# Kernel tuning notes

Measured on AMD Instinct MI355X. Metric: run time of the kernel, lower is better.

Reference implementation:

```python
import jax, jax.numpy as jnp
import numpy as np

N_NODES = 50000
N_EDGES = 800000
N_GRAPHS = 512
VOCAB = 128
HID = 64
NCLS = 5


def _seg_mean(vals, ids, num_segments):
    s = jax.ops.segment_sum(vals, ids, num_segments=num_segments)
    cnt = jax.ops.segment_sum(jnp.ones((vals.shape[0],), vals.dtype), ids, num_segments=num_segments)
    return s / jnp.maximum(cnt, 1.0)[:, None]


def sage_conv(x, src, dst, W_l, b_l, W_r):
    # PyG SAGEConv (mean aggr): out = lin_l(mean_{j in N(i)} x_j) + lin_r(x_i)
    agg = _seg_mean(x[src], dst, x.shape[0])          # [N, H] gather + scatter-mean
    return agg @ W_l.T + b_l + x @ W_r.T


def setup_inputs() -> dict:
    key = jax.random.key(0)
    ks = jax.random.split(key, 10)
    scale = 1.0 / np.sqrt(HID)
    x_tokens = jax.random.randint(ks[0], (N_NODES,), 0, VOCAB)
    edge_index = jax.random.randint(ks[1], (2, N_EDGES), 0, N_NODES)
    batch = jnp.sort(jax.random.randint(ks[2], (N_NODES,), 0, N_GRAPHS))
    return {
        "x_tokens": x_tokens,
        "edge_index": edge_index,
        "batch": batch,
        "embed": jax.random.normal(ks[3], (VOCAB, HID), jnp.float32),
        "W1l": jax.random.normal(ks[4], (HID, HID), jnp.float32) * scale,
        "b1l": jnp.zeros((HID,), jnp.float32),
        "W1r": jax.random.normal(ks[5], (HID, HID), jnp.float32) * scale,
        "W2l": jax.random.normal(ks[6], (HID, HID), jnp.float32) * scale,
        "b2l": jnp.zeros((HID,), jnp.float32),
        "W2r": jax.random.normal(ks[7], (HID, HID), jnp.float32) * scale,
        "Wlin": jax.random.normal(ks[8], (NCLS, HID), jnp.float32) * scale,
        "blin": jnp.zeros((NCLS,), jnp.float32),
    }


def reference(x_tokens, edge_index, batch, embed, W1l, b1l, W1r, W2l, b2l, W2r, Wlin, blin):
    src, dst = edge_index[0], edge_index[1]
    x = embed[x_tokens]                                  # [N, H] embedding lookup
    x = jax.nn.relu(sage_conv(x, src, dst, W1l, b1l, W1r))
    x = jax.nn.relu(sage_conv(x, src, dst, W2l, b2l, W2r))
    g = _seg_mean(x, batch, N_GRAPHS)                    # global_mean_pool -> [G, H]
    return g @ Wlin.T + blin                             # [G, num_classes]
```

## Files before the change

kernel.cpp:

```cpp
#include <hip/hip_runtime.h>

#define N_NODES  50000
#define N_EDGES  800000
#define N_GRAPHS 512
#define HID      64
#define NCLS     5
#define NB       64
#define EST      36
#define AST      68

typedef __attribute__((ext_vector_type(8))) short bf16x8;
typedef __attribute__((ext_vector_type(4))) float f32x4;

__device__ inline unsigned short f2bf(float f) {
    unsigned int u = __builtin_bit_cast(unsigned int, f);
    unsigned int r = (u + 0x7FFFu + ((u >> 16) & 1u)) >> 16;
    return (unsigned short)r;
}
__device__ inline unsigned int packbf(float a, float b) {
    return (unsigned int)f2bf(a) | ((unsigned int)f2bf(b) << 16);
}
__device__ inline float bf2f(unsigned int u16) {
    unsigned int t = u16 << 16;
    return __builtin_bit_cast(float, t);
}

#define EBUF_T (128 * 32)
#define PW_T   (64 * 64)
#define PREP_T (N_EDGES + EBUF_T + N_NODES + 2 * PW_T)
__global__ void k_prep_fill(
    const int* __restrict__ src, const int* __restrict__ dst,
    const int* __restrict__ tok,
    int* __restrict__ cnt, unsigned int* __restrict__ bucket,
    const float* __restrict__ embed, unsigned int* __restrict__ ebufg,
    const int* __restrict__ batch,
    int* __restrict__ pos_start, int* __restrict__ pos_end,
    const float* __restrict__ W1l, const float* __restrict__ W1r,
    unsigned int* __restrict__ wb1,
    const float* __restrict__ W2l, const float* __restrict__ W2r,
    unsigned int* __restrict__ wb2) {
    int gid = blockIdx.x * blockDim.x + threadIdx.x;
    if (gid < N_EDGES) {
        int s = src[gid], d = dst[gid];
        unsigned int t = (unsigned int)tok[s];
        int pos = atomicAdd(&cnt[d], 1);
        if (pos < NB) {
            __builtin_nontemporal_store((unsigned int)s | (t << 16),
                                        &bucket[(long)d * NB + pos]);
        }
        return;
    }
    gid -= N_EDGES;
    if (gid < EBUF_T) {
        int t = gid >> 5, c = gid & 31;
        float2 v = ((const float2*)(embed + (long)t * HID))[c];
        ebufg[gid] = packbf(v.x, v.y);
        return;
    }
    gid -= EBUF_T;
    if (gid < N_NODES) {
        int n = gid;
        int b = batch[n];
        if (n == 0 || batch[n - 1] != b) pos_start[b] = n;
        if (n == N_NODES - 1 || batch[n + 1] != b) pos_end[b] = n + 1;
        return;
    }
    gid -= N_NODES;
    if (gid < 2 * PW_T) {
        const float* Wl = (gid < PW_T) ? W1l : W2l;
        const float* Wr = (gid < PW_T) ? W1r : W2r;
        unsigned int* wb = (gid < PW_T) ? wb1 : wb2;
        int i = (gid < PW_T) ? gid : gid - PW_T;
        int h = i >> 6, c = i & 63;
        float2 v = (c < 32) ? ((const float2*)(Wl + (long)h * HID))[c]
                            : ((const float2*)(Wr + (long)h * HID))[c - 32];
        wb[i] = packbf(v.x, v.y);
    }
}

template <bool L1>
__global__ __launch_bounds__(1024) void k_layer(
    const int* __restrict__ cnt, const unsigned int* __restrict__ bucket,
    const int* __restrict__ tok, const unsigned int* __restrict__ ebufg,
    const unsigned int* __restrict__ xb,
    const unsigned int* __restrict__ wb, const float* __restrict__ bl,
    unsigned short* __restrict__ xoutb)
{
    __shared__ unsigned int As[64 * AST];
    __shared__ unsigned int elds[L1 ? 128 * EST : 1];
    const int tid  = threadIdx.x;
    const int wv   = tid >> 6;
    const int lane = tid & 63;
    const int n0   = blockIdx.x * 64;

    if (L1) {
        for (int i = tid; i < EBUF_T; i += 1024) {
            int t = i >> 5, c = i & 31;
            elds[t * EST + c] = ebufg[i];
        }
        __syncthreads();
    }

    const int q  = lane & 7;
    const int e8 = lane >> 3;

#pragma unroll
    for (int i = 0; i < 4; ++i) {
        int rl = wv * 4 + i;
        int nn = n0 + rl;
        int nc = min(nn, N_NODES - 1);
        int deg = cnt[nc];
        int m   = (nn < N_NODES) ? min(deg, NB) : 0;
        unsigned int v = (lane < m) ? bucket[(long)nc * NB + lane] : 0u;
        float f0 = 0, f1 = 0, f2 = 0, f3 = 0, f4 = 0, f5 = 0, f6 = 0, f7 = 0;
#pragma unroll
        for (int g = 0; g < 8; ++g) {
            int j = g * 8 + e8;
            unsigned int vv = __shfl(v, j, 64);
            if (j < m) {
                uint4 w4;
                if (L1) w4 = *(const uint4*)(elds + (vv >> 16) * EST + q * 4);
                else    w4 = *((const uint4*)(xb + (long)(vv & 0xffffu) * 32) + q);
                f0 += bf2f(w4.x & 0xffff); f1 += bf2f(w4.x >> 16);
                f2 += bf2f(w4.y & 0xffff); f3 += bf2f(w4.y >> 16);
                f4 += bf2f(w4.z & 0xffff); f5 += bf2f(w4.z >> 16);
                f6 += bf2f(w4.w & 0xffff); f7 += bf2f(w4.w >> 16);
            }
        }
#pragma unroll
        for (int o = 8; o < 64; o <<= 1) {
            f0 += __shfl_xor(f0, o, 64); f1 += __shfl_xor(f1, o, 64);
            f2 += __shfl_xor(f2, o, 64); f3 += __shfl_xor(f3, o, 64);
            f4 += __shfl_xor(f4, o, 64); f5 += __shfl_xor(f5, o, 64);
            f6 += __shfl_xor(f6, o, 64); f7 += __shfl_xor(f7, o, 64);
        }
        if (e8 == 0) {
            float inv = 1.0f / (float)max(deg, 1);
            uint4 o;
            o.x = packbf(f0 * inv, f1 * inv);
            o.y = packbf(f2 * inv, f3 * inv);
            o.z = packbf(f4 * inv, f5 * inv);
            o.w = packbf(f6 * inv, f7 * inv);
            *(uint4*)(As + rl * AST + q * 4) = o;
        } else if (e8 == 1) {
            uint4 sv;
            if (L1) { int tk = tok[nc]; sv = *(const uint4*)(elds + tk * EST + q * 4); }
            else    { sv = *((const uint4*)(xb + (long)nc * 32) + q); }
            *(uint4*)(As + rl * AST + 32 + q * 4) = sv;
        }
    }
    __syncthreads();

    const int s    = wv & 3;
    const int t    = wv >> 2;
    const int mm   = lane & 15;
    const int quad = lane >> 4;

    bf16x8 afr[4];
#pragma unroll
    for (int kst = 0; kst < 4; ++kst)
        afr[kst] = *(const bf16x8*)(As + (s * 16 + mm) * AST + kst * 16 + quad * 4);

    f32x4 acc = (f32x4){0.f, 0.f, 0.f, 0.f};
#pragma unroll
    for (int kst = 0; kst < 4; ++kst) {
        bf16x8 bfr = *(const bf16x8*)(wb + (t * 16 + mm) * 64 + kst * 16 + quad * 4);
        acc = __builtin_amdgcn_mfma_f32_16x16x32_bf16(bfr, afr[kst], acc, 0, 0, 0);
    }

    int node = n0 + s * 16 + mm;
    if (node < N_NODES) {
        int hb = t * 16 + quad * 4;
        float4 bb = *(const float4*)(bl + hb);
        ushort4 o;
        o.x = f2bf(fmaxf(acc[0] + bb.x, 0.f));
        o.y = f2bf(fmaxf(acc[1] + bb.y, 0.f));
        o.z = f2bf(fmaxf(acc[2] + bb.z, 0.f));
        o.w = f2bf(fmaxf(acc[3] + bb.w, 0.f));
        *(ushort4*)(xoutb + (long)node * HID + hb) = o;
    }
}

__global__ __launch_bounds__(64) void k_pool(
    const unsigned int* __restrict__ x2b,
    const int* __restrict__ pos_start, const int* __restrict__ pos_end,
    const float* __restrict__ Wlin, const float* __restrict__ blin,
    float* __restrict__ out)
{
    int g    = blockIdx.x;
    int lane = threadIdx.x;
    int q    = lane & 7;
    int slot = lane >> 3;
    int s = pos_start[g], e = pos_end[g];
    float f0 = 0, f1 = 0, f2 = 0, f3 = 0, f4 = 0, f5 = 0, f6 = 0, f7 = 0;
    for (int n = s + slot; n < e; n += 8) {
        uint4 v = *((const uint4*)(x2b + (long)n * 32) + q);
        f0 += bf2f(v.x & 0xffff); f1 += bf2f(v.x >> 16);
        f2 += bf2f(v.y & 0xffff); f3 += bf2f(v.y >> 16);
        f4 += bf2f(v.z & 0xffff); f5 += bf2f(v.z >> 16);
        f6 += bf2f(v.w & 0xffff); f7 += bf2f(v.w >> 16);
    }
#pragma unroll
    for (int o = 8; o < 64; o <<= 1) {
        f0 += __shfl_xor(f0, o, 64); f1 += __shfl_xor(f1, o, 64);
        f2 += __shfl_xor(f2, o, 64); f3 += __shfl_xor(f3, o, 64);
        f4 += __shfl_xor(f4, o, 64); f5 += __shfl_xor(f5, o, 64);
        f6 += __shfl_xor(f6, o, 64); f7 += __shfl_xor(f7, o, 64);
    }
    float inv = 1.0f / (float)max(e - s, 1);
    f0 *= inv; f1 *= inv; f2 *= inv; f3 *= inv;
    f4 *= inv; f5 *= inv; f6 *= inv; f7 *= inv;
#pragma unroll
    for (int c = 0; c < NCLS; ++c) {
        const float* wr = Wlin + c * HID + q * 8;
        float p = f0 * wr[0] + f1 * wr[1] + f2 * wr[2] + f3 * wr[3] +
                  f4 * wr[4] + f5 * wr[5] + f6 * wr[6] + f7 * wr[7];
        p += __shfl_xor(p, 1, 64);
        p += __shfl_xor(p, 2, 64);
        p += __shfl_xor(p, 4, 64);
        if (lane == 0) out[g * NCLS + c] = p + blin[c];
    }
}

extern "C" void kernel_launch(void* const* d_in, const int* in_sizes, int n_in,
                              void* d_out, int out_size, void* d_ws, size_t ws_size,
                              hipStream_t stream) {
    const int*   tok   = (const int*)d_in[0];
    const int*   eidx  = (const int*)d_in[1];
    const int*   batch = (const int*)d_in[2];
    const float* embed = (const float*)d_in[3];
    const float* W1l   = (const float*)d_in[4];
    const float* b1l   = (const float*)d_in[5];
    const float* W1r   = (const float*)d_in[6];
    const float* W2l   = (const float*)d_in[7];
    const float* b2l   = (const float*)d_in[8];
    const float* W2r   = (const float*)d_in[9];
    const float* Wlin  = (const float*)d_in[10];
    const float* blin  = (const float*)d_in[11];
    float* out = (float*)d_out;

    const int* src = eidx;
    const int* dst = eidx + N_EDGES;

    char* wsp = (char*)d_ws;
    size_t off = 0;
    auto alloc = [&](size_t bytes) -> void* {
        void* p = wsp + off;
        off = (off + bytes + 255) & ~(size_t)255;
        return p;
    };
    int*   cnt     = (int*)  alloc((size_t)N_NODES * 4);
    int*   pstart  = (int*)  alloc((size_t)N_GRAPHS * 4);
    int*   pend    = (int*)  alloc((size_t)N_GRAPHS * 4);
    unsigned int* bucket = (unsigned int*)alloc((size_t)N_NODES * NB * 4);
    unsigned int* x1b    = (unsigned int*)alloc((size_t)N_NODES * 32 * 4);
    unsigned int* x2b    = (unsigned int*)alloc((size_t)N_NODES * 32 * 4);
    unsigned int* ebufg  = (unsigned int*)alloc((size_t)128 * 32 * 4);
    unsigned int* wb1    = (unsigned int*)alloc((size_t)64 * 64 * 4);
    unsigned int* wb2    = (unsigned int*)alloc((size_t)64 * 64 * 4);

    hipMemsetAsync(cnt, 0, (char*)pend - (char*)cnt + (size_t)N_GRAPHS * 4, stream);

    k_prep_fill<<<(PREP_T + 255) / 256, 256, 0, stream>>>(
        src, dst, tok, cnt, bucket,
        embed, ebufg, batch, pstart, pend, W1l, W1r, wb1, W2l, W2r, wb2);

    const int LBLK = (N_NODES + 63) / 64;
    k_layer<true><<<LBLK, 1024, 0, stream>>>(cnt, bucket, tok, ebufg, nullptr,
                                             wb1, b1l, (unsigned short*)x1b);
    k_layer<false><<<LBLK, 1024, 0, stream>>>(cnt, bucket, nullptr, nullptr, x1b,
                                              wb2, b2l, (unsigned short*)x2b);

    k_pool<<<N_GRAPHS, 64, 0, stream>>>(x2b, pstart, pend, Wlin, blin, out);
}
```

Baseline: 214.0 us.

## Replace per-node global atomic bucketing with two-pass binned counting sort

Instead of each edge doing a global atomicAdd on its destination node's counter and writing into a padded 50000x64 bucket array, edges are histogrammed per 64-node bin in shared memory, scanned, and scattered into a compact per-bin edge list. Each layer block then rebuilds its 64 node buckets in LDS from that bin's edges. This is meant to remove heavy global atomic contention and the large sparse bucket footprint. The cost is two extra kernel launches, including a single-block scan, and rebuilding the LDS buckets in both layers.

After: 226.9 us. 1.06x slower.

```diff
diff --git a/kernel.cpp b/kernel.cpp
--- a/kernel.cpp
+++ b/kernel.cpp
@@ -5,7 +5,9 @@
 #define N_GRAPHS 512
 #define HID      64
 #define NCLS     5
-#define NB       64
+#define NBIN     782
+#define BB       64
+#define EPB      (N_EDGES / BB)
 #define EST      36
 #define AST      68
 
@@ -27,11 +29,10 @@
 
 #define EBUF_T (128 * 32)
 #define PW_T   (64 * 64)
-#define PREP_T (N_EDGES + EBUF_T + N_NODES + 2 * PW_T)
-__global__ void k_prep_fill(
-    const int* __restrict__ src, const int* __restrict__ dst,
-    const int* __restrict__ tok,
-    int* __restrict__ cnt, unsigned int* __restrict__ bucket,
+#define PREP_T (EBUF_T + N_NODES + 2 * PW_T)
+#define PREP_B ((PREP_T + 255) / 256)
+__global__ __launch_bounds__(256) void k_prep_bin1(
+    const int* __restrict__ dst, int* __restrict__ hist,
     const float* __restrict__ embed, unsigned int* __restrict__ ebufg,
     const int* __restrict__ batch,
     int* __restrict__ pos_start, int* __restrict__ pos_end,
@@ -39,18 +40,19 @@
     unsigned int* __restrict__ wb1,
     const float* __restrict__ W2l, const float* __restrict__ W2r,
     unsigned int* __restrict__ wb2) {
-    int gid = blockIdx.x * blockDim.x + threadIdx.x;
-    if (gid < N_EDGES) {
-        int s = src[gid], d = dst[gid];
-        unsigned int t = (unsigned int)tok[s];
-        int pos = atomicAdd(&cnt[d], 1);
-        if (pos < NB) {
-            __builtin_nontemporal_store((unsigned int)s | (t << 16),
-                                        &bucket[(long)d * NB + pos]);
-        }
+    __shared__ int h[NBIN];
+    if (blockIdx.x < BB) {
+        for (int i = threadIdx.x; i < NBIN; i += 256) h[i] = 0;
+        __syncthreads();
+        int base = blockIdx.x * EPB;
+        for (int i = threadIdx.x; i < EPB; i += 256)
+            atomicAdd(&h[dst[base + i] >> 6], 1);
+        __syncthreads();
+        for (int i = threadIdx.x; i < NBIN; i += 256)
+            hist[blockIdx.x * NBIN + i] = h[i];
         return;
     }
-    gid -= N_EDGES;
+    int gid = (blockIdx.x - BB) * 256 + threadIdx.x;
     if (gid < EBUF_T) {
         int t = gid >> 5, c = gid & 31;
         float2 v = ((const float2*)(embed + (long)t * HID))[c];
@@ -71,35 +73,103 @@
         const float* Wr = (gid < PW_T) ? W1r : W2r;
         unsigned int* wb = (gid < PW_T) ? wb1 : wb2;
         int i = (gid < PW_T) ? gid : gid - PW_T;
-        int h = i >> 6, c = i & 63;
-        float2 v = (c < 32) ? ((const float2*)(Wl + (long)h * HID))[c]
-                            : ((const float2*)(Wr + (long)h * HID))[c - 32];
+        int h2 = i >> 6, c = i & 63;
+        float2 v = (c < 32) ? ((const float2*)(Wl + (long)h2 * HID))[c]
+                            : ((const float2*)(Wr + (long)h2 * HID))[c - 32];
         wb[i] = packbf(v.x, v.y);
+    }
+}
+
+__global__ __launch_bounds__(1024) void k_scan(
+    const int* __restrict__ hist, int* __restrict__ bbase,
+    int* __restrict__ bin_off, int* __restrict__ bin_cnt) {
+    __shared__ int sh[1024];
+    int j = threadIdx.x;
+    int run = 0;
+    if (j < NBIN) {
+#pragma unroll 8
+        for (int b = 0; b < BB; ++b) {
+            bbase[b * NBIN + j] = run;
+            run += hist[b * NBIN + j];
+        }
+    }
+    sh[j] = (j < NBIN) ? run : 0;
+    __syncthreads();
+    for (int o = 1; o < 1024; o <<= 1) {
+        int t = (j >= o) ? sh[j - o] : 0;
+        __syncthreads();
+        sh[j] += t;
+        __syncthreads();
+    }
+    if (j < NBIN) {
+        int off = sh[j] - run;
+        bin_off[j] = off;
+        bin_cnt[j] = run;
+#pragma unroll 8
+        for (int b = 0; b < BB; ++b) bbase[b * NBIN + j] += off;
+    }
+}
+
+__global__ __launch_bounds__(256) void k_bin2(
+    const int* __restrict__ src, const int* __restrict__ dst,
+    const int* __restrict__ tok, const int* __restrict__ bbase,
+    unsigned int* __restrict__ ebin) {
+    __shared__ int base[NBIN];
+    __shared__ int cur[NBIN];
+    for (int i = threadIdx.x; i < NBIN; i += 256) {
+        base[i] = bbase[blockIdx.x * NBIN + i];
+        cur[i] = 0;
+    }
+    __syncthreads();
+    int eb = blockIdx.x * EPB;
+    for (int i = threadIdx.x; i < EPB; i += 256) {
+        int s = src[eb + i], d = dst[eb + i];
+        unsigned int t = (unsigned int)tok[s];
+        int bin = d >> 6;
+        int pos = atomicAdd(&cur[bin], 1);
+        ebin[base[bin] + pos] =
+            (unsigned int)s | ((unsigned int)(d & 63) << 16) | (t << 22);
     }
 }
 
 template <bool L1>
 __global__ __launch_bounds__(1024) void k_layer(
-    const int* __restrict__ cnt, const unsigned int* __restrict__ bucket,
+    const int* __restrict__ bin_off, const int* __restrict__ bin_cnt,
+    const unsigned int* __restrict__ ebin,
     const int* __restrict__ tok, const unsigned int* __restrict__ ebufg,
     const unsigned int* __restrict__ xb,
     const unsigned int* __restrict__ wb, const float* __restrict__ bl,
     unsigned short* __restrict__ xoutb)
 {
     __shared__ unsigned int As[64 * AST];
+    __shared__ unsigned int lbucket[64 * 64];
+    __shared__ int lcnt[64];
     __shared__ unsigned int elds[L1 ? 128 * EST : 1];
     const int tid  = threadIdx.x;
     const int wv   = tid >> 6;
     const int lane = tid & 63;
     const int n0   = blockIdx.x * 64;
 
+    if (tid < 64) lcnt[tid] = 0;
     if (L1) {
         for (int i = tid; i < EBUF_T; i += 1024) {
             int t = i >> 5, c = i & 31;
             elds[t * EST + c] = ebufg[i];
         }
-        __syncthreads();
-    }
+    }
+    __syncthreads();
+
+    {
+        int boffv = bin_off[blockIdx.x];
+        int bcnt  = bin_cnt[blockIdx.x];
+        for (int i = tid; i < bcnt; i += 1024) {
+            unsigned int v = ebin[boffv + i];
+            int dl = (v >> 16) & 63;
+            int pos = atomicAdd(&lcnt[dl], 1);
+            if (pos < 64) lbucket[dl * 64 + pos] = v;
+        }
+    }
+    __syncthreads();
 
     const int q  = lane & 7;
     const int e8 = lane >> 3;
@@ -109,9 +179,9 @@
         int rl = wv * 4 + i;
         int nn = n0 + rl;
         int nc = min(nn, N_NODES - 1);
-        int deg = cnt[nc];
-        int m   = (nn < N_NODES) ? min(deg, NB) : 0;
-        unsigned int v = (lane < m) ? bucket[(long)nc * NB + lane] : 0u;
+        int deg = lcnt[rl];
+        int m   = min(deg, 64);
+        unsigned int v = (lane < m) ? lbucket[rl * 64 + lane] : 0u;
         float f0 = 0, f1 = 0, f2 = 0, f3 = 0, f4 = 0, f5 = 0, f6 = 0, f7 = 0;
 #pragma unroll
         for (int g = 0; g < 8; ++g) {
@@ -119,7 +189,7 @@
             unsigned int vv = __shfl(v, j, 64);
             if (j < m) {
                 uint4 w4;
-                if (L1) w4 = *(const uint4*)(elds + (vv >> 16) * EST + q * 4);
+                if (L1) w4 = *(const uint4*)(elds + (vv >> 22) * EST + q * 4);
                 else    w4 = *((const uint4*)(xb + (long)(vv & 0xffffu) * 32) + q);
                 f0 += bf2f(w4.x & 0xffff); f1 += bf2f(w4.x >> 16);
                 f2 += bf2f(w4.y & 0xffff); f3 += bf2f(w4.y >> 16);
@@ -249,27 +319,33 @@
         off = (off + bytes + 255) & ~(size_t)255;
         return p;
     };
-    int*   cnt     = (int*)  alloc((size_t)N_NODES * 4);
     int*   pstart  = (int*)  alloc((size_t)N_GRAPHS * 4);
     int*   pend    = (int*)  alloc((size_t)N_GRAPHS * 4);
-    unsigned int* bucket = (unsigned int*)alloc((size_t)N_NODES * NB * 4);
-    unsigned int* x1b    = (unsigned int*)alloc((size_t)N_NODES * 32 * 4);
-    unsigned int* x2b    = (unsigned int*)alloc((size_t)N_NODES * 32 * 4);
-    unsigned int* ebufg  = (unsigned int*)alloc((size_t)128 * 32 * 4);
-    unsigned int* wb1    = (unsigned int*)alloc((size_t)64 * 64 * 4);
-    unsigned int* wb2    = (unsigned int*)alloc((size_t)64 * 64 * 4);
-
-    hipMemsetAsync(cnt, 0, (char*)pend - (char*)cnt + (size_t)N_GRAPHS * 4, stream);
-
-    k_prep_fill<<<(PREP_T + 255) / 256, 256, 0, stream>>>(
-        src, dst, tok, cnt, bucket,
-        embed, ebufg, batch, pstart, pend, W1l, W1r, wb1, W2l, W2r, wb2);
-
-    const int LBLK = (N_NODES + 63) / 64;
-    k_layer<true><<<LBLK, 1024, 0, stream>>>(cnt, bucket, tok, ebufg, nullptr,
-                                             wb1, b1l, (unsigned short*)x1b);
-    k_layer<false><<<LBLK, 1024, 0, stream>>>(cnt, bucket, nullptr, nullptr, x1b,
-                                              wb2, b2l, (unsigned short*)x2b);
+    int*   hist    = (int*)  alloc((size_t)BB * NBIN * 4);
+    int*   bbase   = (int*)  alloc((size_t)BB * NBIN * 4);
+    int*   bin_off = (int*)  alloc((size_t)NBIN * 4);
+    int*   bin_cnt = (int*)  alloc((size_t)NBIN * 4);
+    unsigned int* ebin  = (unsigned int*)alloc((size_t)N_EDGES * 4);
+    unsigned int* x1b   = (unsigned int*)alloc((size_t)N_NODES * 32 * 4);
+    unsigned int* x2b   = (unsigned int*)alloc((size_t)N_NODES * 32 * 4);
+    unsigned int* ebufg = (unsigned int*)alloc((size_t)128 * 32 * 4);
+    unsigned int* wb1   = (unsigned int*)alloc((size_t)64 * 64 * 4);
+    unsigned int* wb2   = (unsigned int*)alloc((size_t)64 * 64 * 4);
+
+    hipMemsetAsync(pstart, 0, (char*)pend - (char*)pstart + (size_t)N_GRAPHS * 4, stream);
+
+    k_prep_bin1<<<BB + PREP_B, 256, 0, stream>>>(
+        dst, hist, embed, ebufg, batch, pstart, pend,
+        W1l, W1r, wb1, W2l, W2r, wb2);
+
+    k_scan<<<1, 1024, 0, stream>>>(hist, bbase, bin_off, bin_cnt);
+    k_bin2<<<BB, 256, 0, stream>>>(src, dst, tok, bbase, ebin);
+
+    const int LBLK = NBIN;
+    k_layer<true><<<LBLK, 1024, 0, stream>>>(bin_off, bin_cnt, ebin, tok, ebufg,
+                                             nullptr, wb1, b1l, (unsigned short*)x1b);
+    k_layer<false><<<LBLK, 1024, 0, stream>>>(bin_off, bin_cnt, ebin, nullptr, nullptr,
+                                              x1b, wb2, b2l, (unsigned short*)x2b);
 
     k_pool<<<N_GRAPHS, 64, 0, stream>>>(x2b, pstart, pend, Wlin, blin, out);
 }
```
